# Performance work log

Measured on AMD Instinct MI355X. Metric: run time of the kernel, lower is better.

## Reference

```python
import jax, jax.numpy as jnp
import numpy as np

THRESHOLD = 0.5
PSI_ZONE = 0.1


def dequantize_ternary(w, threshold=THRESHOLD, psi_zone=PSI_ZONE):
    """Faithful reproduction of TernaryTensor.from_float followed by to_float.

    Branch order matches the original code:
      v > threshold        -> +1
      v < -threshold       -> -1
      |v| < psi_zone       -> 0
      otherwise (PSI)      -> (v + threshold) / (2 * threshold)  (stored psi_prob)
    """
    psi_val = (w + threshold) / (2.0 * threshold)
    return jnp.where(
        w > threshold, 1.0,
        jnp.where(
            w < -threshold, -1.0,
            jnp.where(jnp.abs(w) < psi_zone, 0.0, psi_val),
        ),
    ).astype(w.dtype)


def setup_inputs() -> dict:
    key = jax.random.key(0)
    k_x, k_w = jax.random.split(key)
    batch, in_features, out_features = 8192, 4096, 4096
    x = jax.random.normal(k_x, (batch, in_features), dtype=jnp.float32)
    # original: torch.randn(out, in) * 0.1
    weight_float = jax.random.normal(k_w, (out_features, in_features), dtype=jnp.float32) * 0.1
    bias = jnp.zeros((out_features,), dtype=jnp.float32)
    return {"x": x, "weight_float": weight_float, "bias": bias}


def reference(x, weight_float, bias):
    w = dequantize_ternary(weight_float)  # [out, in]
    return jnp.matmul(x, w.T) + bias      # [batch, out]
```

## Files before the change

kernel.cpp:

```cpp
#include <hip/hip_runtime.h>
#include <stdint.h>

#define THRESH 0.5f
#define PSI 0.1f

typedef short bfrag_t __attribute__((ext_vector_type(8)));
typedef float f32x16 __attribute__((ext_vector_type(16)));
typedef unsigned short u16x8 __attribute__((ext_vector_type(8)));

#define GLD16(gsrc, ldst)                                                                \
    __builtin_amdgcn_global_load_lds((const __attribute__((address_space(1))) void*)(gsrc), \
                                     (__attribute__((address_space(3))) void*)(ldst),       \
                                     16, 0, 0)

#define WAITVM(n) asm volatile("s_waitcnt vmcnt(" #n ")" ::: "memory")
#define BAR()                                  \
    do {                                       \
        asm volatile("" ::: "memory");         \
        __builtin_amdgcn_s_barrier();          \
        asm volatile("" ::: "memory");         \
    } while (0)

__device__ __forceinline__ float dequant(float v) {
    if (v > THRESH) return 1.0f;
    if (v < -THRESH) return -1.0f;
    if (fabsf(v) < PSI) return 0.0f;
    return (v + THRESH) / (2.0f * THRESH);
}

__device__ __forceinline__ unsigned short f2bf(float f) {
    unsigned int u = __float_as_uint(f);
    u += 0x7FFFu + ((u >> 16) & 1u);
    return (unsigned short)(u >> 16);
}

__global__ void quantW_kernel(const float* __restrict__ w, unsigned short* __restrict__ wb, int n8) {
    const int stride = gridDim.x * blockDim.x;
    for (int i = blockIdx.x * blockDim.x + threadIdx.x; i < n8; i += stride) {
        const float4* p = (const float4*)w + (size_t)i * 2;
        float4 a = p[0], b = p[1];
        u16x8 o;
        o[0] = f2bf(dequant(a.x)); o[1] = f2bf(dequant(a.y));
        o[2] = f2bf(dequant(a.z)); o[3] = f2bf(dequant(a.w));
        o[4] = f2bf(dequant(b.x)); o[5] = f2bf(dequant(b.y));
        o[6] = f2bf(dequant(b.z)); o[7] = f2bf(dequant(b.w));
        *(u16x8*)(wb + (size_t)i * 8) = o;
    }
}

__global__ void cvtX_kernel(const float* __restrict__ x, unsigned short* __restrict__ xb, int n8) {
    const int stride = gridDim.x * blockDim.x;
    for (int i = blockIdx.x * blockDim.x + threadIdx.x; i < n8; i += stride) {
        const float4* p = (const float4*)x + (size_t)i * 2;
        float4 a = p[0], b = p[1];
        u16x8 o;
        o[0] = f2bf(a.x); o[1] = f2bf(a.y); o[2] = f2bf(a.z); o[3] = f2bf(a.w);
        o[4] = f2bf(b.x); o[5] = f2bf(b.y); o[6] = f2bf(b.z); o[7] = f2bf(b.w);
        *(u16x8*)(xb + (size_t)i * 8) = o;
    }
}


__device__ __forceinline__ bfrag_t rdfrag32(const char* halfBase, int band, int ks, int l16) {
    return *(const bfrag_t*)(halfBase + (band << 11) + (ks << 10) + l16);
}

__device__ __forceinline__ void mfma_half(f32x16 (&acc)[4][2], int mbase,
                                          const bfrag_t (&a)[2][2], const bfrag_t (&b)[2][2]) {
#pragma unroll
    for (int ks = 0; ks < 2; ++ks)
#pragma unroll
        for (int mi = 0; mi < 2; ++mi)
#pragma unroll
            for (int nn = 0; nn < 2; ++nn)
                acc[mbase + mi][nn] = __builtin_amdgcn_mfma_f32_32x32x16_bf16(
                    a[mi][ks], b[nn][ks], acc[mbase + mi][nn], 0, 0, 0);
}

__global__ __launch_bounds__(512, 2) void gemm256_kernel(
        const unsigned short* __restrict__ A,
        const unsigned short* __restrict__ B,
        const float* __restrict__ bias,
        float* __restrict__ C,
        int M, int N, int K) {
    __shared__ unsigned short lds[65536];
    char* ldsB = (char*)lds;

    const int t    = threadIdx.x;
    const int w    = t >> 6;
    const int l    = t & 63;
    const int wr   = w >> 2;
    const int wc   = w & 3;
    const int lr32 = l & 31;
    const int hi   = l >> 5;
    const int l16  = l << 4;

    const int nwg = gridDim.x;
    int bid = blockIdx.x;
    if ((nwg & 7) == 0) bid = (bid & 7) * (nwg >> 3) + (bid >> 3);
    const int nbn  = N >> 8;
    const int brow = (bid / nbn) << 8;
    const int bcol = (bid % nbn) << 8;

    const int c16a = w * 2 + 0, c16b = w * 2 + 1;
    const int rowA = ((c16a >> 1) << 5) + lr32;
    const int rowB = ((c16b >> 1) << 5) + lr32;
    const int kelA = ((c16a & 1) << 4) + (hi << 3);
    const int kelB = ((c16b & 1) << 4) + (hi << 3);

    const unsigned short* aS0 = A + (size_t)(brow + rowA) * K + kelA;
    const unsigned short* aS1 = A + (size_t)(brow + rowB) * K + kelB;
    const unsigned short* bS0 = B + (size_t)(bcol + rowA) * K + kelA;
    const unsigned short* bS1 = B + (size_t)(bcol + rowB) * K + kelB;

#define STAGE_A(buf, half, kE)                                                              \
    do {                                                                                    \
        GLD16(aS0 + (kE) + (half) * 32, ldsB + (buf) * 65536 + (half) * 16384 + c16a * 1024); \
        GLD16(aS1 + (kE) + (half) * 32, ldsB + (buf) * 65536 + (half) * 16384 + c16b * 1024); \
    } while (0)
#define STAGE_B(buf, half, kE)                                                              \
    do {                                                                                    \
        GLD16(bS0 + (kE) + (half) * 32, ldsB + (buf) * 65536 + 32768 + (half) * 16384 + c16a * 1024); \
        GLD16(bS1 + (kE) + (half) * 32, ldsB + (buf) * 65536 + 32768 + (half) * 16384 + c16b * 1024); \
    } while (0)

    f32x16 acc[4][2];
#pragma unroll
    for (int m = 0; m < 4; ++m)
#pragma unroll
        for (int n = 0; n < 2; ++n)
#pragma unroll
            for (int r = 0; r < 16; ++r)
                acc[m][n][r] = 0.f;

    const int NT = K >> 6;
    const int wrB4 = wr << 2;
    const int wcB2 = wc << 1;
    const int wrBase = wr << 7;
    const int wcBase = wc << 6;

    {
        const int k1 = (NT > 1) ? 64 : 0;
        STAGE_A(0, 0, 0); STAGE_B(0, 0, 0);
        STAGE_A(0, 1, 0); STAGE_B(0, 1, 0);
        STAGE_A(1, 0, k1); STAGE_B(1, 0, k1);
        WAITVM(4);
        BAR();
    }

    for (int tt = 0; tt < NT; ++tt) {
        const int X = tt & 1, Y = X ^ 1;
        const char* aH0 = ldsB + X * 65536;
        const char* aH1 = aH0 + 16384;
        const char* bH0 = aH0 + 32768;
        const char* bH1 = aH0 + 49152;
        int t1 = tt + 1; if (t1 >= NT) t1 -= NT;
        int t2 = tt + 2; if (t2 >= NT) t2 -= NT;
        const int kY1 = t1 << 6;
        const int kX2 = t2 << 6;

        bfrag_t a[2][2], b[2][2];

#pragma unroll
        for (int mi = 0; mi < 2; ++mi)
#pragma unroll
            for (int ks = 0; ks < 2; ++ks)
                a[mi][ks] = rdfrag32(aH0, wrB4 + mi, ks, l16);
#pragma unroll
        for (int nn = 0; nn < 2; ++nn)
#pragma unroll
            for (int ks = 0; ks < 2; ++ks)
                b[nn][ks] = rdfrag32(bH0, wcB2 + nn, ks, l16);
        STAGE_A(Y, 1, kY1);
        BAR();
        __builtin_amdgcn_s_setprio(1);
        mfma_half(acc, 0, a, b);
        __builtin_amdgcn_s_setprio(0);
        BAR();

#pragma unroll
        for (int mi = 0; mi < 2; ++mi)
#pragma unroll
            for (int ks = 0; ks < 2; ++ks)
                a[mi][ks] = rdfrag32(aH0, wrB4 + 2 + mi, ks, l16);
        STAGE_B(Y, 1, kY1);
        BAR();
        __builtin_amdgcn_s_setprio(1);
        mfma_half(acc, 2, a, b);
        __builtin_amdgcn_s_setprio(0);
        WAITVM(8);
        BAR();

#pragma unroll
        for (int mi = 0; mi < 2; ++mi)
#pragma unroll
            for (int ks = 0; ks < 2; ++ks)
                a[mi][ks] = rdfrag32(aH1, wrB4 + mi, ks, l16);
#pragma unroll
        for (int nn = 0; nn < 2; ++nn)
#pragma unroll
            for (int ks = 0; ks < 2; ++ks)
                b[nn][ks] = rdfrag32(bH1, wcB2 + nn, ks, l16);
        STAGE_A(X, 0, kX2);
        BAR();
        __builtin_amdgcn_s_setprio(1);
        mfma_half(acc, 0, a, b);
        __builtin_amdgcn_s_setprio(0);
        BAR();

#pragma unroll
        for (int mi = 0; mi < 2; ++mi)
#pragma unroll
            for (int ks = 0; ks < 2; ++ks)
                a[mi][ks] = rdfrag32(aH1, wrB4 + 2 + mi, ks, l16);
        STAGE_B(X, 0, kX2);
        BAR();
        __builtin_amdgcn_s_setprio(1);
        mfma_half(acc, 2, a, b);
        __builtin_amdgcn_s_setprio(0);
        WAITVM(8);
        BAR();
    }

    WAITVM(0);

    float bv[2];
#pragma unroll
    for (int nn = 0; nn < 2; ++nn) bv[nn] = bias[bcol + wcBase + nn * 32 + lr32];
#pragma unroll
    for (int mm = 0; mm < 4; ++mm) {
#pragma unroll
        for (int nn = 0; nn < 2; ++nn) {
            const int gc = bcol + wcBase + nn * 32 + lr32;
#pragma unroll
            for (int reg = 0; reg < 16; ++reg) {
                const int row = (reg & 3) + 8 * (reg >> 2) + 4 * hi;
                C[(size_t)(brow + wrBase + mm * 32 + row) * N + gc] = acc[mm][nn][reg] + bv[nn];
            }
        }
    }
    (void)M;
#undef STAGE_A
#undef STAGE_B
}

__global__ void gemm_fallback_kernel(const float* __restrict__ X, const float* __restrict__ W,
                                     const float* __restrict__ bias, float* __restrict__ C,
                                     int M, int N, int K) {
    __shared__ float sX[16][17];
    __shared__ float sW[16][17];
    const int tx = threadIdx.x & 15;
    const int ty = threadIdx.x >> 4;
    const int row = blockIdx.y * 16 + ty;
    const int colBase = blockIdx.x * 16;
    const int col = colBase + tx;
    float acc = 0.f;
    for (int k0 = 0; k0 < K; k0 += 16) {
        sX[ty][tx] = (row < M && k0 + tx < K) ? X[(size_t)row * K + k0 + tx] : 0.f;
        const int wrow = colBase + ty;
        sW[ty][tx] = (wrow < N && k0 + tx < K) ? dequant(W[(size_t)wrow * K + k0 + tx]) : 0.f;
        __syncthreads();
#pragma unroll
        for (int kk = 0; kk < 16; ++kk)
            acc += sX[ty][kk] * sW[tx][kk];
        __syncthreads();
    }
    if (row < M && col < N)
        C[(size_t)row * N + col] = acc + bias[col];
}

extern "C" void kernel_launch(void* const* d_in, const int* in_sizes, int n_in,
                              void* d_out, int out_size, void* d_ws, size_t ws_size,
                              hipStream_t stream) {
    const float* x    = (const float*)d_in[0];
    const float* w    = (const float*)d_in[1];
    const float* bias = (const float*)d_in[2];
    float* out        = (float*)d_out;

    const int N = in_sizes[2];
    const int K = in_sizes[1] / N;
    const int M = in_sizes[0] / K;

    const size_t need = ((size_t)M * K + (size_t)N * K) * sizeof(unsigned short);
    const bool fast = (ws_size >= need) && (M % 256 == 0) && (N % 256 == 0) && (K % 64 == 0) && (K >= 128);

    if (fast) {
        unsigned short* xb = (unsigned short*)d_ws;
        unsigned short* wb = xb + (size_t)M * K;
        cvtX_kernel<<<dim3(2048), dim3(256), 0, stream>>>(x, xb, (M * K) / 8);
        quantW_kernel<<<dim3(2048), dim3(256), 0, stream>>>(w, wb, (N * K) / 8);
        gemm256_kernel<<<dim3((M / 256) * (N / 256)), dim3(512), 0, stream>>>(xb, wb, bias, out, M, N, K);
    } else {
        dim3 g((N + 15) / 16, (M + 15) / 16);
        gemm_fallback_kernel<<<g, dim3(256), 0, stream>>>(x, w, bias, out, M, N, K);
    }
    (void)n_in; (void)out_size;
}
```

Baseline: 334.6 us.

## Pre-pack bf16 operands into LDS-tile order so GEMM loads are contiguous

```diff
diff --git a/kernel.cpp b/kernel.cpp
--- a/kernel.cpp
+++ b/kernel.cpp
@@ -34,30 +34,45 @@
     return (unsigned short)(u >> 16);
 }
 
-__global__ void quantW_kernel(const float* __restrict__ w, unsigned short* __restrict__ wb, int n8) {
-    const int stride = gridDim.x * blockDim.x;
-    for (int i = blockIdx.x * blockDim.x + threadIdx.x; i < n8; i += stride) {
-        const float4* p = (const float4*)w + (size_t)i * 2;
-        float4 a = p[0], b = p[1];
+template <bool DO_DEQUANT>
+__global__ void pack_kernel(const float* __restrict__ src, unsigned short* __restrict__ dst, int K) {
+    __shared__ char lsm[16384];
+    const int t   = threadIdx.x;
+    const int nkc = K >> 8;
+    const int b   = blockIdx.x / nkc;
+    const int kc  = blockIdx.x % nkc;
+    const int k0  = kc << 8;
+    const int r   = t >> 3;
+    const int j   = t & 7;
+
+    const float4* s4 = (const float4*)(src + (size_t)((b << 5) + r) * K + k0 + (j << 5));
+    float4 f[8];
+#pragma unroll
+    for (int i = 0; i < 8; ++i) f[i] = s4[i];
+
+#pragma unroll
+    for (int gi = 0; gi < 4; ++gi) {
+        float4 lo = f[2 * gi], hi4 = f[2 * gi + 1];
         u16x8 o;
-        o[0] = f2bf(dequant(a.x)); o[1] = f2bf(dequant(a.y));
-        o[2] = f2bf(dequant(a.z)); o[3] = f2bf(dequant(a.w));
-        o[4] = f2bf(dequant(b.x)); o[5] = f2bf(dequant(b.y));
-        o[6] = f2bf(dequant(b.z)); o[7] = f2bf(dequant(b.w));
-        *(u16x8*)(wb + (size_t)i * 8) = o;
-    }
-}
-
-__global__ void cvtX_kernel(const float* __restrict__ x, unsigned short* __restrict__ xb, int n8) {
-    const int stride = gridDim.x * blockDim.x;
-    for (int i = blockIdx.x * blockDim.x + threadIdx.x; i < n8; i += stride) {
-        const float4* p = (const float4*)x + (size_t)i * 2;
-        float4 a = p[0], b = p[1];
-        u16x8 o;
-        o[0] = f2bf(a.x); o[1] = f2bf(a.y); o[2] = f2bf(a.z); o[3] = f2bf(a.w);
-        o[4] = f2bf(b.x); o[5] = f2bf(b.y); o[6] = f2bf(b.z); o[7] = f2bf(b.w);
-        *(u16x8*)(xb + (size_t)i * 8) = o;
-    }
+        if (DO_DEQUANT) {
+            o[0] = f2bf(dequant(lo.x));  o[1] = f2bf(dequant(lo.y));
+            o[2] = f2bf(dequant(lo.z));  o[3] = f2bf(dequant(lo.w));
+            o[4] = f2bf(dequant(hi4.x)); o[5] = f2bf(dequant(hi4.y));
+            o[6] = f2bf(dequant(hi4.z)); o[7] = f2bf(dequant(hi4.w));
+        } else {
+            o[0] = f2bf(lo.x);  o[1] = f2bf(lo.y);  o[2] = f2bf(lo.z);  o[3] = f2bf(lo.w);
+            o[4] = f2bf(hi4.x); o[5] = f2bf(hi4.y); o[6] = f2bf(hi4.z); o[7] = f2bf(hi4.w);
+        }
+        const int S_rel = 2 * j + (gi >> 1);
+        const int slot  = ((gi & 1) << 5) + r;
+        *(u16x8*)(lsm + S_rel * 1024 + slot * 16) = o;
+    }
+    __syncthreads();
+
+    unsigned short* gdst = dst + (((size_t)b * (K >> 4) + (kc << 4)) << 9) + (size_t)t * 32;
+#pragma unroll
+    for (int i = 0; i < 4; ++i)
+        *(u16x8*)(gdst + i * 8) = *(const u16x8*)(lsm + t * 64 + i * 16);
 }
 
 
@@ -78,8 +93,8 @@
 }
 
 __global__ __launch_bounds__(512, 2) void gemm256_kernel(
-        const unsigned short* __restrict__ A,
-        const unsigned short* __restrict__ B,
+        const unsigned short* __restrict__ Ap,
+        const unsigned short* __restrict__ Bp,
         const float* __restrict__ bias,
         float* __restrict__ C,
         int M, int N, int K) {
@@ -102,26 +117,22 @@
     const int brow = (bid / nbn) << 8;
     const int bcol = (bid % nbn) << 8;
 
+    const int Kc = K >> 4;
+    const char* pA = (const char*)Ap + (((size_t)(((brow >> 5) + w) * (size_t)Kc)) << 10) + l16;
+    const char* pB = (const char*)Bp + (((size_t)(((bcol >> 5) + w) * (size_t)Kc)) << 10) + l16;
     const int c16a = w * 2 + 0, c16b = w * 2 + 1;
-    const int rowA = ((c16a >> 1) << 5) + lr32;
-    const int rowB = ((c16b >> 1) << 5) + lr32;
-    const int kelA = ((c16a & 1) << 4) + (hi << 3);
-    const int kelB = ((c16b & 1) << 4) + (hi << 3);
-
-    const unsigned short* aS0 = A + (size_t)(brow + rowA) * K + kelA;
-    const unsigned short* aS1 = A + (size_t)(brow + rowB) * K + kelB;
-    const unsigned short* bS0 = B + (size_t)(bcol + rowA) * K + kelA;
-    const unsigned short* bS1 = B + (size_t)(bcol + rowB) * K + kelB;
 
 #define STAGE_A(buf, half, kE)                                                              \
     do {                                                                                    \
-        GLD16(aS0 + (kE) + (half) * 32, ldsB + (buf) * 65536 + (half) * 16384 + c16a * 1024); \
-        GLD16(aS1 + (kE) + (half) * 32, ldsB + (buf) * 65536 + (half) * 16384 + c16b * 1024); \
+        const size_t so_ = ((size_t)(((kE) >> 4) + (half) * 2)) << 10;                      \
+        GLD16(pA + so_,        ldsB + (buf) * 65536 + (half) * 16384 + c16a * 1024);        \
+        GLD16(pA + so_ + 1024, ldsB + (buf) * 65536 + (half) * 16384 + c16b * 1024);        \
     } while (0)
 #define STAGE_B(buf, half, kE)                                                              \
     do {                                                                                    \
-        GLD16(bS0 + (kE) + (half) * 32, ldsB + (buf) * 65536 + 32768 + (half) * 16384 + c16a * 1024); \
-        GLD16(bS1 + (kE) + (half) * 32, ldsB + (buf) * 65536 + 32768 + (half) * 16384 + c16b * 1024); \
+        const size_t so_ = ((size_t)(((kE) >> 4) + (half) * 2)) << 10;                      \
+        GLD16(pB + so_,        ldsB + (buf) * 65536 + 32768 + (half) * 16384 + c16a * 1024);\
+        GLD16(pB + so_ + 1024, ldsB + (buf) * 65536 + 32768 + (half) * 16384 + c16b * 1024);\
     } while (0)
 
     f32x16 acc[4][2];
@@ -282,14 +293,15 @@
     const int M = in_sizes[0] / K;
 
     const size_t need = ((size_t)M * K + (size_t)N * K) * sizeof(unsigned short);
-    const bool fast = (ws_size >= need) && (M % 256 == 0) && (N % 256 == 0) && (K % 64 == 0) && (K >= 128);
+    const bool fast = (ws_size >= need) && (M % 256 == 0) && (N % 256 == 0) &&
+                      (K % 256 == 0);
 
     if (fast) {
-        unsigned short* xb = (unsigned short*)d_ws;
-        unsigned short* wb = xb + (size_t)M * K;
-        cvtX_kernel<<<dim3(2048), dim3(256), 0, stream>>>(x, xb, (M * K) / 8);
-        quantW_kernel<<<dim3(2048), dim3(256), 0, stream>>>(w, wb, (N * K) / 8);
-        gemm256_kernel<<<dim3((M / 256) * (N / 256)), dim3(512), 0, stream>>>(xb, wb, bias, out, M, N, K);
+        unsigned short* xp = (unsigned short*)d_ws;
+        unsigned short* wp = xp + (size_t)M * K;
+        pack_kernel<false><<<dim3((M / 32) * (K / 256)), dim3(256), 0, stream>>>(x, xp, K);
+        pack_kernel<true ><<<dim3((N / 32) * (K / 256)), dim3(256), 0, stream>>>(w, wp, K);
+        gemm256_kernel<<<dim3((M / 256) * (N / 256)), dim3(512), 0, stream>>>(xp, wp, bias, out, M, N, K);
     } else {
         dim3 g((N + 15) / 16, (M + 15) / 16);
         gemm_fallback_kernel<<<g, dim3(256), 0, stream>>>(x, w, bias, out, M, N, K);
```

After: 286.2 us. 14.5% less time.
